# Kernel optimization log

Measured on AMD Instinct MI355X. Metric: run time of the kernel, lower is better.

The kernel has to match this reference:

```python
import jax, jax.numpy as jnp
import numpy as np

N_NODES = 50000
DEG = 16                      # uniform in-degree so every node receives messages (matches dgl mailbox semantics)
N_EDGES = N_NODES * DEG       # 800000
IND = 128
EDIM = 64
OUT = 128
AVG_D = float(np.log(DEG + 1.0))   # PNA avg_d['log']
EPS = 1e-5


def setup_inputs() -> dict:
    key = jax.random.key(0)
    k = jax.random.split(key, 6)
    h = jax.random.normal(k[0], (N_NODES, IND), dtype=jnp.float32)
    ef = jax.random.normal(k[1], (N_EDGES, EDIM), dtype=jnp.float32)
    src = jax.random.randint(k[2], (N_EDGES,), 0, N_NODES)
    dst = jnp.repeat(jnp.arange(N_NODES), DEG)  # every node has exactly DEG incoming edges
    pre_in = 2 * IND + EDIM            # 320
    post_in = IND * (1 + 4 * 3)        # 1664: h + 4 aggregators x 3 scalers
    W_pre = jax.random.normal(k[3], (pre_in, IND), dtype=jnp.float32) * (1.0 / np.sqrt(pre_in))
    b_pre = jnp.zeros((IND,), dtype=jnp.float32)
    W_post = jax.random.normal(k[4], (post_in, OUT), dtype=jnp.float32) * (1.0 / np.sqrt(post_in))
    b_post = jnp.zeros((OUT,), dtype=jnp.float32)
    return {"h": h, "ef": ef, "src": src, "dst": dst,
            "W_pre": W_pre, "b_pre": b_pre, "W_post": W_post, "b_post": b_post}


def reference(h, ef, src, dst, W_pre, b_pre, W_post, b_post):
    n = h.shape[0]
    # --- pretrans on edges: cat(src_h, dst_h, ef) -> Linear ---
    z2 = jnp.concatenate([h[src], h[dst], ef], axis=1)          # [E, 2*IND+EDIM]
    e = z2 @ W_pre + b_pre                                       # [E, IND]
    # --- multi-aggregator segment reduce over incoming edges (by dst) ---
    deg = jax.ops.segment_sum(jnp.ones((e.shape[0],), e.dtype), dst, num_segments=n)  # [N]
    safe_deg = jnp.maximum(deg, 1.0)[:, None]
    s1 = jax.ops.segment_sum(e, dst, num_segments=n)
    s2 = jax.ops.segment_sum(e * e, dst, num_segments=n)
    mean = s1 / safe_deg
    std = jnp.sqrt(jax.nn.relu(s2 / safe_deg - mean * mean) + EPS)
    mx = jax.ops.segment_max(e, dst, num_segments=n)
    mn = jax.ops.segment_min(e, dst, num_segments=n)
    has = (deg > 0)[:, None]
    mx = jnp.where(has, mx, 0.0)
    mn = jnp.where(has, mn, 0.0)
    agg = jnp.concatenate([mean, mx, mn, std], axis=1)           # [N, 4*IND]
    # --- scalers: identity, amplification log(D+1)/avg_d, attenuation avg_d/log(D+1) ---
    logd = jnp.log(deg + 1.0)
    amp = (logd / AVG_D)[:, None]
    att = (AVG_D / jnp.maximum(logd, 1e-6))[:, None]
    att = jnp.where(deg[:, None] > 0, att, 0.0)
    scaled = jnp.concatenate([agg, agg * amp, agg * att], axis=1)  # [N, 12*IND]
    # --- posttrans on nodes: cat(h, aggregated) -> Linear ---
    hcat = jnp.concatenate([h, scaled], axis=1)                  # [N, 13*IND]
    return hcat @ W_post + b_post                                # [N, OUT]
```

## Files before the change

### kernel.cpp

```cpp
#include <hip/hip_runtime.h>

#define N_NODES 50000
#define IND 128
#define EDIM 64

typedef __bf16 bf16x8 __attribute__((ext_vector_type(8)));
typedef float  f32x4  __attribute__((ext_vector_type(4)));
typedef unsigned short u16x8 __attribute__((ext_vector_type(8)));

__device__ __forceinline__ unsigned short f2bfu(float f) {
  __bf16 b = (__bf16)f;
  return __builtin_bit_cast(unsigned short, b);
}
__device__ __forceinline__ float bfu2f(unsigned short u) {
  __bf16 b = __builtin_bit_cast(__bf16, u);
  return (float)b;
}
__device__ __forceinline__ f32x4 mfma16(bf16x8 a, bf16x8 b, f32x4 c) {
  return __builtin_amdgcn_mfma_f32_16x16x32_bf16(a, b, c, 0, 0, 0);
}
__device__ __forceinline__ bf16x8 pack8(float4 a, float4 b) {
  bf16x8 r;
  r[0]=(__bf16)a.x; r[1]=(__bf16)a.y; r[2]=(__bf16)a.z; r[3]=(__bf16)a.w;
  r[4]=(__bf16)b.x; r[5]=(__bf16)b.y; r[6]=(__bf16)b.z; r[7]=(__bf16)b.w;
  return r;
}

__global__ __launch_bounds__(256) void pack_all(const float* W_pre, const float* W_post,
                                                const float* b_pre, const float* b_post,
                                                unsigned short* WpreF, unsigned short* WcF,
                                                unsigned short* WfoldF, float* bias2) {
  __shared__ float ldsW[16384];
  int b = blockIdx.x, t = threadIdx.x;
  if (b < 16) {
    for (int i = 0; i < 64; i++) {
      int idx = t + i * 256;
      int c = idx >> 7, col = idx & 127;
      float s = 0.f;
#pragma unroll
      for (int sc = 0; sc < 3; sc++)
#pragma unroll
      for (int st = 0; st < 3; st++)
          s += W_post[(size_t)(128 + sc * 512 + st * 128 + c) * 128 + col];
      ldsW[idx] = s;
    }
    __syncthreads();
    int col = t & 127, kh = t >> 7;
    for (int i = 0; i < 4; i++) {
      int k = b * 8 + i * 2 + kh;
      float a0 = W_post[(size_t)k * 128 + col], a1 = 0.f, a2 = 0.f, a3 = 0.f;
      const float* wb = W_pre + (size_t)(128 + k) * 128;
#pragma unroll 4
      for (int c = 0; c < 128; c += 4) {
        a0 = fmaf(wb[c],     ldsW[c * 128 + col], a0);
        a1 = fmaf(wb[c + 1], ldsW[(c + 1) * 128 + col], a1);
        a2 = fmaf(wb[c + 2], ldsW[(c + 2) * 128 + col], a2);
        a3 = fmaf(wb[c + 3], ldsW[(c + 3) * 128 + col], a3);
      }
      float acc = (a0 + a1) + (a2 + a3);
      int kb = k >> 5, j = k & 7, qq = (k >> 3) & 3;
      int lane = qq * 16 + (col & 15), ct = col >> 4;
      WfoldF[((size_t)(kb * 8 + ct) * 64 + lane) * 8 + j] = f2bfu(acc);
    }
    if (b == 0 && t < 128) {
      int col = t;
      float acc = b_post[col];
      for (int c = 0; c < 128; c++) acc = fmaf(b_pre[c], ldsW[c * 128 + col], acc);
      bias2[col] = acc;
    }
  } else {
    int idx = (b - 16) * 256 + t;
    if (idx < 16384) {
      int j = idx & 7, lane = (idx >> 3) & 63, ct = (idx >> 9) & 7, kb = idx >> 12;
      int k = kb * 32 + (lane >> 4) * 8 + j;
      int col = ct * 16 + (lane & 15);
      WpreF[idx] = f2bfu(W_pre[k * 128 + col]);
    } else if (idx < 24576) {
      int i = idx - 16384;
      int j = i & 7, lane = (i >> 3) & 63, ct = (i >> 9) & 7, kb = i >> 12;
      int k = kb * 32 + (lane >> 4) * 8 + j;
      int col = ct * 16 + (lane & 15);
      WcF[i] = f2bfu(W_pre[(256 + k) * 128 + col]);
    } else if (idx < 24576 + 65536) {
      int i = idx - 24576;
      int j = i & 7, lane = (i >> 3) & 63, ct = (i >> 9) & 7, kbr = i >> 12;
      int kb = kbr + 4;
      int p = kbr * 32 + ((lane >> 4) & 3) * 8 + j;
      int tt = p >> 7;
      int c = (p & 7) * 16 + ((p >> 3) & 15);
      int col = ct * 16 + (lane & 15);
      size_t r0 = 128 + (size_t)tt * 128 + c;
      float v = W_post[r0 * 128 + col] + W_post[(r0 + 512) * 128 + col] +
                W_post[(r0 + 1024) * 128 + col];
      WfoldF[((size_t)(kb * 8 + ct) * 64 + lane) * 8 + j] = f2bfu(v);
    }
  }
}

__global__ __launch_bounds__(256) void pre_gemm(const float* h, const unsigned short* WpreF,
                                                unsigned short* haB) {
  int lane = threadIdx.x & 63;
  int gw = blockIdx.x * 4 + (threadIdx.x >> 6);
  size_t base = (size_t)gw * 16;
  if (base >= N_NODES) return;
  int q = lane >> 4, c16 = lane & 15;
  f32x4 acc[8];
#pragma unroll
  for (int i = 0; i < 8; i++) acc[i] = (f32x4){0.f, 0.f, 0.f, 0.f};
#pragma unroll
  for (int kb = 0; kb < 4; kb++) {
    const float* hp = h + (base + c16) * 128 + kb * 32 + q * 8;
    float4 lo = *(const float4*)hp;
    float4 hi = *(const float4*)(hp + 4);
    bf16x8 a = pack8(lo, hi);
#pragma unroll
    for (int ct = 0; ct < 8; ct++) {
      bf16x8 b = *(const bf16x8*)(WpreF + ((size_t)(kb * 8 + ct) * 64 + lane) * 8);
      acc[ct] = mfma16(a, b, acc[ct]);
    }
  }
#pragma unroll
  for (int r = 0; r < 4; r++) {
    size_t row = base + q * 4 + r;
    u16x8 hv;
#pragma unroll
    for (int ct = 0; ct < 8; ct++) hv[ct] = f2bfu(acc[ct][r]);
    *(u16x8*)(haB + row * 128 + c16 * 8) = hv;
  }
}

__device__ __forceinline__ void node_stats(const f32x4* acc, const u16x8* G,
                                           int q, unsigned short* outp) {
  u16x8 ov;
#pragma unroll
  for (int ct = 0; ct < 8; ct++) {
    float sum = 0.f, s2 = 0.f, mx = -3.4e38f, mn = 3.4e38f;
#pragma unroll
    for (int r = 0; r < 4; r++) {
      float e = acc[ct][r] + bfu2f(G[r][ct]);
      sum += e; s2 = __builtin_fmaf(e, e, s2);
      mx = fmaxf(mx, e); mn = fminf(mn, e);
    }
    sum += __shfl_xor(sum, 16, 64); s2 += __shfl_xor(s2, 16, 64);
    mx = fmaxf(mx, __shfl_xor(mx, 16, 64)); mn = fminf(mn, __shfl_xor(mn, 16, 64));
    sum += __shfl_xor(sum, 32, 64); s2 += __shfl_xor(s2, 32, 64);
    mx = fmaxf(mx, __shfl_xor(mx, 32, 64)); mn = fminf(mn, __shfl_xor(mn, 32, 64));
    float mean = sum * 0.0625f;
    float var = fmaxf(s2 * 0.0625f - mean * mean, 0.f);
    float sd = sqrtf(var + 1e-5f);
    float v = (q == 0) ? mean : (q == 1) ? mx : (q == 2) ? mn : sd;
    ov[ct] = f2bfu(v);
  }
  *(u16x8*)outp = ov;
}

__global__ __launch_bounds__(256, 4) void edge_agg(const float* ef, const int* src,
                                                   const unsigned short* haB,
                                                   const unsigned short* WcF,
                                                   unsigned short* aggB) {
  __shared__ unsigned short ldsWc[8192];
  {
    const int4* g = (const int4*)WcF;
    int4* l = (int4*)ldsWc;
#pragma unroll
    for (int i = 0; i < 4; i++) l[threadIdx.x + i * 256] = g[threadIdx.x + i * 256];
  }
  int lane = threadIdx.x & 63, wib = threadIdx.x >> 6;
  int q = lane >> 4, c16 = lane & 15;
  int pr = blockIdx.x * 4 + wib;
  int n0 = pr * 2;
  int srcv = src[pr * 32 + (lane & 31)];
  const float* ep0 = ef + ((size_t)n0 * 16 + c16) * 64 + q * 8;
  float4 E0a = *(const float4*)ep0;
  float4 E0b = *(const float4*)(ep0 + 4);
  float4 E0c = *(const float4*)(ep0 + 32);
  float4 E0d = *(const float4*)(ep0 + 36);
  const float* ep1 = ep0 + 1024;
  float4 E1a = *(const float4*)ep1;
  float4 E1b = *(const float4*)(ep1 + 4);
  float4 E1c = *(const float4*)(ep1 + 32);
  float4 E1d = *(const float4*)(ep1 + 36);
  u16x8 G0[4], G1[4];
#pragma unroll
  for (int r = 0; r < 4; r++) {
    int s = __shfl(srcv, q * 4 + r, 64);
    G0[r] = *(const u16x8*)(haB + (size_t)s * 128 + c16 * 8);
  }
#pragma unroll
  for (int r = 0; r < 4; r++) {
    int s = __shfl(srcv, 16 + q * 4 + r, 64);
    G1[r] = *(const u16x8*)(haB + (size_t)s * 128 + c16 * 8);
  }
  __syncthreads();
  {
    bf16x8 a0 = pack8(E0a, E0b), a1 = pack8(E0c, E0d);
    f32x4 acc[8];
#pragma unroll
    for (int ct = 0; ct < 8; ct++) {
      bf16x8 b = *(const bf16x8*)(ldsWc + ((size_t)ct * 64 + lane) * 8);
      acc[ct] = mfma16(a0, b, (f32x4){0.f, 0.f, 0.f, 0.f});
    }
#pragma unroll
    for (int ct = 0; ct < 8; ct++) {
      bf16x8 b = *(const bf16x8*)(ldsWc + ((size_t)(8 + ct) * 64 + lane) * 8);
      acc[ct] = mfma16(a1, b, acc[ct]);
    }
    node_stats(acc, G0, q, aggB + (size_t)n0 * 512 + lane * 8);
  }
  {
    bf16x8 a0 = pack8(E1a, E1b), a1 = pack8(E1c, E1d);
    f32x4 acc[8];
#pragma unroll
    for (int ct = 0; ct < 8; ct++) {
      bf16x8 b = *(const bf16x8*)(ldsWc + ((size_t)ct * 64 + lane) * 8);
      acc[ct] = mfma16(a0, b, (f32x4){0.f, 0.f, 0.f, 0.f});
    }
#pragma unroll
    for (int ct = 0; ct < 8; ct++) {
      bf16x8 b = *(const bf16x8*)(ldsWc + ((size_t)(8 + ct) * 64 + lane) * 8);
      acc[ct] = mfma16(a1, b, acc[ct]);
    }
    node_stats(acc, G1, q, aggB + (size_t)(n0 + 1) * 512 + lane * 8);
  }
}

__global__ __launch_bounds__(256, 4) void post_gemm(const float* h, const unsigned short* aggB,
                                                    const unsigned short* WfoldF,
                                                    const float* bias2, float* out) {
  int lane = threadIdx.x & 63;
  int gw = blockIdx.x * 4 + (threadIdx.x >> 6);
  size_t base = (size_t)gw * 16;
  if (base >= N_NODES) return;
  int q = lane >> 4, c16 = lane & 15;
  size_t r0 = base + c16;
  f32x4 acc[8];
#pragma unroll
  for (int i = 0; i < 8; i++) acc[i] = (f32x4){0.f, 0.f, 0.f, 0.f};
  float4 fa, fb; u16x8 ua;
  {
    const float* p = h + r0 * 128 + q * 8;
    fa = *(const float4*)p; fb = *(const float4*)(p + 4);
  }
  bf16x8 Bc[8], Bn[8];
#pragma unroll
  for (int ct = 0; ct < 8; ct++)
    Bc[ct] = *(const bf16x8*)(WfoldF + ((size_t)ct * 64 + lane) * 8);
#pragma unroll
  for (int kb = 0; kb < 20; kb++) {
    bf16x8 a = (kb < 4) ? pack8(fa, fb) : __builtin_bit_cast(bf16x8, ua);
    if (kb + 1 < 4) {
      const float* p = h + r0 * 128 + (kb + 1) * 32 + q * 8;
      fa = *(const float4*)p; fb = *(const float4*)(p + 4);
    } else if (kb + 1 < 20) {
      ua = *(const u16x8*)(aggB + r0 * 512 + (size_t)(kb + 1 - 4) * 32 + q * 8);
    }
    if (kb + 1 < 20) {
#pragma unroll
      for (int ct = 0; ct < 8; ct++)
        Bn[ct] = *(const bf16x8*)(WfoldF + ((size_t)((kb + 1) * 8 + ct) * 64 + lane) * 8);
    }
#pragma unroll
    for (int ct = 0; ct < 8; ct++) acc[ct] = mfma16(a, Bc[ct], acc[ct]);
#pragma unroll
    for (int ct = 0; ct < 8; ct++) Bc[ct] = Bn[ct];
  }
#pragma unroll
  for (int ct = 0; ct < 8; ct++) {
    int col = ct * 16 + c16;
    float bp = bias2[col];
#pragma unroll
    for (int r = 0; r < 4; r++) {
      size_t row = base + q * 4 + r;
      out[row * 128 + col] = acc[ct][r] + bp;
    }
  }
}

extern "C" void kernel_launch(void* const* d_in, const int* in_sizes, int n_in,
                              void* d_out, int out_size, void* d_ws, size_t ws_size,
                              hipStream_t stream) {
  const float* h      = (const float*)d_in[0];
  const float* ef     = (const float*)d_in[1];
  const int*   src    = (const int*)d_in[2];
  const float* W_pre  = (const float*)d_in[4];
  const float* b_pre  = (const float*)d_in[5];
  const float* W_post = (const float*)d_in[6];
  const float* b_post = (const float*)d_in[7];
  float* out = (float*)d_out;

  char* ws = (char*)d_ws;
  unsigned short* haB    = (unsigned short*)ws;
  unsigned short* aggB   = haB + (size_t)N_NODES * 128;
  unsigned short* WpreF  = aggB + (size_t)N_NODES * 512;
  unsigned short* WcF    = WpreF + 16384;
  unsigned short* WfoldF = WcF + 8192;
  float*          bias2  = (float*)(WfoldF + 81920);
  (void)in_sizes; (void)n_in; (void)out_size; (void)ws_size;

  pack_all<<<368, 256, 0, stream>>>(W_pre, W_post, b_pre, b_post, WpreF, WcF, WfoldF, bias2);
  pre_gemm<<<782, 256, 0, stream>>>(h, WpreF, haB);
  edge_agg<<<6250, 256, 0, stream>>>(ef, src, haB, WcF, aggB);
  post_gemm<<<782, 256, 0, stream>>>(h, aggB, WfoldF, bias2, out);
}
```

Baseline: 399.6 us.

## Fuse edge aggregation with post-transform GEMM through shared memory

```diff
diff --git a/kernel.cpp b/kernel.cpp
--- a/kernel.cpp
+++ b/kernel.cpp
@@ -154,20 +154,23 @@
   *(u16x8*)outp = ov;
 }
 
-__global__ __launch_bounds__(256, 4) void edge_agg(const float* ef, const int* src,
-                                                   const unsigned short* haB,
-                                                   const unsigned short* WcF,
-                                                   unsigned short* aggB) {
+__global__ __launch_bounds__(512, 4) void edge_post(const float* ef, const int* src,
+                                                    const unsigned short* haB,
+                                                    const unsigned short* WcF,
+                                                    const float* h,
+                                                    const unsigned short* WfoldF,
+                                                    const float* bias2, float* out) {
   __shared__ unsigned short ldsWc[8192];
+  __shared__ unsigned short sAgg[16 * 512];
   {
     const int4* g = (const int4*)WcF;
     int4* l = (int4*)ldsWc;
 #pragma unroll
-    for (int i = 0; i < 4; i++) l[threadIdx.x + i * 256] = g[threadIdx.x + i * 256];
+    for (int i = 0; i < 2; i++) l[threadIdx.x + i * 512] = g[threadIdx.x + i * 512];
   }
   int lane = threadIdx.x & 63, wib = threadIdx.x >> 6;
   int q = lane >> 4, c16 = lane & 15;
-  int pr = blockIdx.x * 4 + wib;
+  int pr = blockIdx.x * 8 + wib;
   int n0 = pr * 2;
   int srcv = src[pr * 32 + (lane & 31)];
   const float* ep0 = ef + ((size_t)n0 * 16 + c16) * 64 + q * 8;
@@ -205,7 +208,7 @@
       bf16x8 b = *(const bf16x8*)(ldsWc + ((size_t)(8 + ct) * 64 + lane) * 8);
       acc[ct] = mfma16(a1, b, acc[ct]);
     }
-    node_stats(acc, G0, q, aggB + (size_t)n0 * 512 + lane * 8);
+    node_stats(acc, G0, q, sAgg + (size_t)(wib * 2) * 512 + lane * 8);
   }
   {
     bf16x8 a0 = pack8(E1a, E1b), a1 = pack8(E1c, E1d);
@@ -220,59 +223,42 @@
       bf16x8 b = *(const bf16x8*)(ldsWc + ((size_t)(8 + ct) * 64 + lane) * 8);
       acc[ct] = mfma16(a1, b, acc[ct]);
     }
-    node_stats(acc, G1, q, aggB + (size_t)(n0 + 1) * 512 + lane * 8);
-  }
-}
-
-__global__ __launch_bounds__(256, 4) void post_gemm(const float* h, const unsigned short* aggB,
-                                                    const unsigned short* WfoldF,
-                                                    const float* bias2, float* out) {
-  int lane = threadIdx.x & 63;
-  int gw = blockIdx.x * 4 + (threadIdx.x >> 6);
-  size_t base = (size_t)gw * 16;
-  if (base >= N_NODES) return;
-  int q = lane >> 4, c16 = lane & 15;
+    node_stats(acc, G1, q, sAgg + (size_t)(wib * 2 + 1) * 512 + lane * 8);
+  }
+  __syncthreads();
+  size_t base = (size_t)blockIdx.x * 16;
   size_t r0 = base + c16;
-  f32x4 acc[8];
-#pragma unroll
-  for (int i = 0; i < 8; i++) acc[i] = (f32x4){0.f, 0.f, 0.f, 0.f};
-  float4 fa, fb; u16x8 ua;
+  f32x4 acc = (f32x4){0.f, 0.f, 0.f, 0.f};
+  float4 fa, fb;
   {
     const float* p = h + r0 * 128 + q * 8;
     fa = *(const float4*)p; fb = *(const float4*)(p + 4);
   }
-  bf16x8 Bc[8], Bn[8];
-#pragma unroll
-  for (int ct = 0; ct < 8; ct++)
-    Bc[ct] = *(const bf16x8*)(WfoldF + ((size_t)ct * 64 + lane) * 8);
+  bf16x8 Bc = *(const bf16x8*)(WfoldF + ((size_t)wib * 64 + lane) * 8);
 #pragma unroll
   for (int kb = 0; kb < 20; kb++) {
-    bf16x8 a = (kb < 4) ? pack8(fa, fb) : __builtin_bit_cast(bf16x8, ua);
-    if (kb + 1 < 4) {
-      const float* p = h + r0 * 128 + (kb + 1) * 32 + q * 8;
-      fa = *(const float4*)p; fb = *(const float4*)(p + 4);
-    } else if (kb + 1 < 20) {
-      ua = *(const u16x8*)(aggB + r0 * 512 + (size_t)(kb + 1 - 4) * 32 + q * 8);
-    }
-    if (kb + 1 < 20) {
-#pragma unroll
-      for (int ct = 0; ct < 8; ct++)
-        Bn[ct] = *(const bf16x8*)(WfoldF + ((size_t)((kb + 1) * 8 + ct) * 64 + lane) * 8);
-    }
-#pragma unroll
-    for (int ct = 0; ct < 8; ct++) acc[ct] = mfma16(a, Bc[ct], acc[ct]);
-#pragma unroll
-    for (int ct = 0; ct < 8; ct++) Bc[ct] = Bn[ct];
-  }
-#pragma unroll
-  for (int ct = 0; ct < 8; ct++) {
-    int col = ct * 16 + c16;
-    float bp = bias2[col];
-#pragma unroll
-    for (int r = 0; r < 4; r++) {
-      size_t row = base + q * 4 + r;
-      out[row * 128 + col] = acc[ct][r] + bp;
-    }
+    bf16x8 a;
+    if (kb < 4) {
+      a = pack8(fa, fb);
+      if (kb < 3) {
+        const float* p = h + r0 * 128 + (kb + 1) * 32 + q * 8;
+        fa = *(const float4*)p; fb = *(const float4*)(p + 4);
+      }
+    } else {
+      a = *(const bf16x8*)(sAgg + (size_t)c16 * 512 + (kb - 4) * 32 + q * 8);
+    }
+    bf16x8 Bn = Bc;
+    if (kb < 19)
+      Bn = *(const bf16x8*)(WfoldF + ((size_t)((kb + 1) * 8 + wib) * 64 + lane) * 8);
+    acc = mfma16(a, Bc, acc);
+    Bc = Bn;
+  }
+  int col = wib * 16 + c16;
+  float bp = bias2[col];
+#pragma unroll
+  for (int r = 0; r < 4; r++) {
+    size_t row = base + q * 4 + r;
+    out[row * 128 + col] = acc[r] + bp;
   }
 }
 
@@ -290,8 +276,7 @@
 
   char* ws = (char*)d_ws;
   unsigned short* haB    = (unsigned short*)ws;
-  unsigned short* aggB   = haB + (size_t)N_NODES * 128;
-  unsigned short* WpreF  = aggB + (size_t)N_NODES * 512;
+  unsigned short* WpreF  = haB + (size_t)N_NODES * 128;
   unsigned short* WcF    = WpreF + 16384;
   unsigned short* WfoldF = WcF + 8192;
   float*          bias2  = (float*)(WfoldF + 81920);
@@ -299,6 +284,5 @@
 
   pack_all<<<368, 256, 0, stream>>>(W_pre, W_post, b_pre, b_post, WpreF, WcF, WfoldF, bias2);
   pre_gemm<<<782, 256, 0, stream>>>(h, WpreF, haB);
-  edge_agg<<<6250, 256, 0, stream>>>(ef, src, haB, WcF, aggB);
-  post_gemm<<<782, 256, 0, stream>>>(h, aggB, WfoldF, bias2, out);
-}
+  edge_post<<<3125, 512, 0, stream>>>(ef, src, haB, WcF, h, WfoldF, bias2, out);
+}
```

New measurement: 397.5 us. No clear change (-0.5%).
